# Optimization experiments

Measured on AMD Instinct MI355X. Metric: run time of the kernel, lower is better.

The kernel has to match this reference:

```python
import jax, jax.numpy as jnp
import numpy as np

B, N, C = 8, 196, 512
NC, H = 10, 8
HD = C // H
SCALE = HD ** -0.5


def setup_inputs() -> dict:
    key = jax.random.key(0)
    ks = jax.random.split(key, 8)
    s = 1.0 / np.sqrt(C)
    return {
        "x": jax.random.normal(ks[0], (B, N, C), jnp.float32),
        "anchors": jax.random.normal(ks[1], (NC, N, C), jnp.float32),
        "weights": jax.random.uniform(ks[2], (B, H, NC), jnp.float32),
        "Wqk": jax.random.normal(ks[3], (C, C), jnp.float32) * s,
        "Wqk2": jax.random.normal(ks[4], (C, C), jnp.float32) * s,
        "Wv": jax.random.normal(ks[5], (C, C), jnp.float32) * s,
        "Wproj": jax.random.normal(ks[6], (C, C), jnp.float32) * s,
        "bproj": jax.random.normal(ks[7], (C,), jnp.float32) * 0.01,
    }


def _heads(t):
    # (..., N, C) -> (..., H, N, HD)
    shp = t.shape[:-2]
    return t.reshape(shp + (t.shape[-2], H, HD)).swapaxes(-3, -2)


def reference(x, anchors, weights, Wqk, Wqk2, Wv, Wproj, bproj):
    v = _heads(x @ Wv)                      # (B, H, N, HD)
    q = _heads(x @ Wqk)[:, None]            # (B, 1, H, N, HD)
    k = _heads(anchors @ Wqk)[None]         # (1, NC, H, N, HD)
    q2 = _heads(x @ Wqk2)[:, None]          # (B, 1, H, N, HD)
    k2 = _heads(anchors @ Wqk2)[None]       # (1, NC, H, N, HD)

    # ReLU-clipped double attention, both (B, NC, H, N, N)
    left_attn = jnp.maximum(-(q @ k.swapaxes(-2, -1)) * SCALE, 0.0)
    right_attn = jnp.maximum((k2 @ q2.swapaxes(-2, -1)) * SCALE, 0.0)

    attn = left_attn @ right_attn           # (B, NC, H, N, N)
    # per-head class-weighted combine: (B,H,NC) x (B,NC,H,N,N) -> (B,H,N,N)
    tmp = jnp.einsum('bhc,bchnm->bhnm', weights, attn)
    out = tmp @ v                           # (B, H, N, HD)
    # NOTE: original torch code reshapes (B,H,N,HD)->(B,N,C) WITHOUT a
    # transpose back; we replicate that exact flatten order.
    out = out.reshape(B, N, C)
    out = out @ Wproj + bproj
    return (out, left_attn)
```

## Files before the change

kernel.cpp:

```cpp
#include <hip/hip_runtime.h>

#define OFF_XB     0u
#define OFF_AB     1605632u
#define OFF_WQKT   3612672u
#define OFF_WQK2T  4136960u
#define OFF_WVT    4661248u
#define OFF_WPROJT 5185536u
#define OFF_XQ     5709824u
#define OFF_XQ2    7315456u
#define OFF_AQ     8921088u
#define OFF_AQ2    10928128u
#define OFF_XVT    12935168u
#define OFF_WRVT   14639104u
#define OFF_OUT1   36265984u

typedef __attribute__((ext_vector_type(8))) short bf16x8;
typedef __attribute__((ext_vector_type(4))) float f32x4;
#define MFMA(a, b, c) __builtin_amdgcn_mfma_f32_16x16x32_bf16((a), (b), (c), 0, 0, 0)

__device__ __forceinline__ unsigned short f2bf(float x) {
  unsigned u = __builtin_bit_cast(unsigned, x);
  u += 0x7fffu + ((u >> 16) & 1u);
  return (unsigned short)(u >> 16);
}

__device__ __forceinline__ void gl_lds16(const void* g, void* l) {
  __builtin_amdgcn_global_load_lds(
      (const __attribute__((address_space(1))) unsigned int*)g,
      (__attribute__((address_space(3))) unsigned int*)l, 16, 0, 0);
}

__device__ __forceinline__ void stage128(const unsigned short* g0, int stride,
                                         unsigned short (*T)[72], int tid) {
  char* base = (char*)&T[0][0];
  int wv = tid >> 6;
#pragma unroll
  for (int i = 0; i < 4; i++) {
    int k = i * 256 + tid;
    int r = k / 9, c = k - r * 9;
    gl_lds16(g0 + (size_t)r * stride + (c << 3), base + (((i << 2) + wv) << 10));
  }
  if (tid < 128) {
    int k = 1024 + tid;
    int r = k / 9, c = k - r * 9;
    gl_lds16(g0 + (size_t)r * stride + (c << 3), base + ((16 + wv) << 10));
  }
}

__device__ __forceinline__ void stage64x128(const unsigned short* g0, int stride,
                                            unsigned short (*T)[136], int tid) {
  char* base = (char*)&T[0][0];
  int wv = tid >> 6;
#pragma unroll
  for (int i = 0; i < 4; i++) {
    int k = i * 256 + tid;
    int r = k / 17, c = k - r * 17;
    gl_lds16(g0 + (size_t)r * stride + (c << 3), base + (((i << 2) + wv) << 10));
  }
  if (tid < 64) {
    int k = 1024 + tid;
    int r = k / 17, c = k - r * 17;
    gl_lds16(g0 + (size_t)r * stride + (c << 3), base + (16 << 10));
  }
}

__device__ __forceinline__ void stage64(const unsigned short* g0, int stride,
                                        unsigned short (*T)[72], int tid) {
  int wv = tid >> 6;
  char* base = (char*)&T[0][0];
#pragma unroll
  for (int i = 0; i < 2; i++) {
    int k = i * 256 + tid;
    int r = k / 9, c = k - r * 9;
    gl_lds16(g0 + (size_t)r * stride + (c << 3), base + (((i << 2) + wv) << 10));
  }
  if (tid < 64) {
    int k = 512 + tid;
    int r = k / 9, c = k - r * 9;
    gl_lds16(g0 + (size_t)r * stride + (c << 3), base + 8192);
  }
}

__global__ __launch_bounds__(256) void pre_kernel(const float* __restrict__ x, const float* __restrict__ anchors,
                                                  const float* __restrict__ Wqk, const float* __restrict__ Wqk2,
                                                  const float* __restrict__ Wv, const float* __restrict__ Wproj,
                                                  char* __restrict__ ws) {
  int tid = threadIdx.x;
  if (blockIdx.x < 1764) {
    int base = blockIdx.x * 1024 + (tid << 2);
    float4 f = (base < 802816) ? *(const float4*)(x + base)
                               : *(const float4*)(anchors + (base - 802816));
    unsigned short s[4] = {f2bf(f.x), f2bf(f.y), f2bf(f.z), f2bf(f.w)};
    *(uint2*)((unsigned short*)(ws + OFF_XB) + base) = *(uint2*)s;
    return;
  }
  __shared__ unsigned short Ls[64][72];
  int idx = blockIdx.x - 1764;
  int wsel = idx >> 6, t = idx & 63;
  int k0 = (t >> 3) << 6, n0 = (t & 7) << 6;
  const float* W;
  unsigned short* WT;
  switch (wsel) {
    case 0:  W = Wqk;   WT = (unsigned short*)(ws + OFF_WQKT);   break;
    case 1:  W = Wqk2;  WT = (unsigned short*)(ws + OFF_WQK2T);  break;
    case 2:  W = Wv;    WT = (unsigned short*)(ws + OFF_WVT);    break;
    default: W = Wproj; WT = (unsigned short*)(ws + OFF_WPROJT); break;
  }
  {
    int r = tid >> 2, seg = (tid & 3) << 4;
    const float* p = W + (size_t)(k0 + r) * 512 + n0 + seg;
    float4 f0 = *(const float4*)p, f1 = *(const float4*)(p + 4);
    float4 f2 = *(const float4*)(p + 8), f3 = *(const float4*)(p + 12);
    unsigned short s[16] = {f2bf(f0.x), f2bf(f0.y), f2bf(f0.z), f2bf(f0.w),
                            f2bf(f1.x), f2bf(f1.y), f2bf(f1.z), f2bf(f1.w),
                            f2bf(f2.x), f2bf(f2.y), f2bf(f2.z), f2bf(f2.w),
                            f2bf(f3.x), f2bf(f3.y), f2bf(f3.z), f2bf(f3.w)};
    *(uint4*)&Ls[r][seg] = *(uint4*)s;
    *(uint4*)&Ls[r][seg + 8] = *(uint4*)(s + 8);
  }
  __syncthreads();
  {
    int r = tid >> 2, seg = (tid & 3) << 4;
    unsigned short s[16];
#pragma unroll
    for (int u = 0; u < 16; u++) s[u] = Ls[seg + u][r];
    unsigned short* dst = WT + (size_t)(n0 + r) * 512 + k0 + seg;
    *(uint4*)dst = *(uint4*)s;
    *(uint4*)(dst + 8) = *(uint4*)(s + 8);
  }
}

__global__ __launch_bounds__(256) void proj5(char* __restrict__ ws) {
  __shared__ unsigned short As[128][72];
  __shared__ unsigned short Bsh[128][72];
  const unsigned short* A;
  const unsigned short* Bp;
  unsigned short* O;
  int M, ostride, row0, col0;
  int z = blockIdx.z;
  if (z < 4) {
    row0 = blockIdx.x << 7;
    col0 = blockIdx.y << 7;
    ostride = 512;
    if (z < 2) { A = (const unsigned short*)(ws + OFF_XB); M = 1568; if (blockIdx.x >= 13) return; }
    else       { A = (const unsigned short*)(ws + OFF_AB); M = 1960; }
    Bp = (const unsigned short*)(ws + ((z & 1) ? OFF_WQK2T : OFF_WQKT));
    O  = (unsigned short*)(ws + (z == 0 ? OFF_XQ : z == 1 ? OFF_XQ2 : z == 2 ? OFF_AQ : OFF_AQ2));
  } else {
    if (blockIdx.x >= 13) return;
    row0 = blockIdx.y << 7;
    col0 = blockIdx.x << 7;
    A = (const unsigned short*)(ws + OFF_WVT);
    Bp = (const unsigned short*)(ws + OFF_XB);
    O = (unsigned short*)(ws + OFF_XVT);
    M = 512; ostride = 1664;
  }
  int tid = threadIdx.x;
  int w = tid >> 6, lm = tid & 15, lq = (tid >> 4) & 3;
  int h1 = w & 1, h2 = w >> 1;
  f32x4 acc[4][4] = {};
  for (int k0 = 0; k0 < 512; k0 += 64) {
    __syncthreads();
    stage128(A + (size_t)row0 * 512 + k0, 512, As, tid);
    stage128(Bp + (size_t)col0 * 512 + k0, 512, Bsh, tid);
    __syncthreads();
#pragma unroll
    for (int kk = 0; kk < 2; kk++) {
      bf16x8 bfr[4];
#pragma unroll
      for (int ni = 0; ni < 4; ni++)
        bfr[ni] = *(const bf16x8*)&Bsh[(h2 << 6) + (ni << 4) + lm][(kk << 5) + (lq << 3)];
#pragma unroll
      for (int mi = 0; mi < 4; mi++) {
        bf16x8 afr = *(const bf16x8*)&As[(h1 << 6) + (mi << 4) + lm][(kk << 5) + (lq << 3)];
#pragma unroll
        for (int ni = 0; ni < 4; ni++) acc[mi][ni] = MFMA(afr, bfr[ni], acc[mi][ni]);
      }
    }
  }
#pragma unroll
  for (int mi = 0; mi < 4; mi++)
#pragma unroll
    for (int r = 0; r < 4; r++) {
      int row = row0 + (h1 << 6) + (mi << 4) + (lq << 2) + r;
      if (row < M) {
#pragma unroll
        for (int ni = 0; ni < 4; ni++) {
          int col = col0 + (h2 << 6) + (ni << 4) + lm;
          O[(size_t)row * ostride + col] = f2bf(acc[mi][ni][r]);
        }
      }
    }
}

__global__ __launch_bounds__(256) void rv2(char* __restrict__ ws, const float* __restrict__ weights) {
  const unsigned short* xq2 = (const unsigned short*)(ws + OFF_XQ2);
  const unsigned short* aq2 = (const unsigned short*)(ws + OFF_AQ2);
  const unsigned short* xvt = (const unsigned short*)(ws + OFF_XVT);
  unsigned short* wrvt      = (unsigned short*)(ws + OFF_WRVT);
  __shared__ unsigned short Bs[128][72];
  __shared__ unsigned short Ss[128][136];
  __shared__ unsigned short Vt[64][136];
  int jblk = blockIdx.x, bch = blockIdx.y;
  int h = bch & 7, bc = bch >> 3;
  int c = bc % 10, b = bc / 10;
  int bh = b * 8 + h;
  int tid = threadIdx.x;
  int w = tid >> 6, lm = tid & 15, lq = (tid >> 4) & 3;
  int h1 = w & 1, h2 = w >> 1;
  float wc = weights[bh * 10 + c];

  stage128(aq2 + (size_t)(c * 196 + jblk * 128) * 512 + (h << 6), 512, Bs, tid);
  __syncthreads();
  bf16x8 af[4][2];
#pragma unroll
  for (int mi = 0; mi < 4; mi++)
#pragma unroll
    for (int kk = 0; kk < 2; kk++)
      af[mi][kk] = *(const bf16x8*)&Bs[(h1 << 6) + (mi << 4) + lm][(kk << 5) + (lq << 3)];

  f32x4 acc[4][2] = {};
  for (int mt = 0; mt < 2; mt++) {
    __syncthreads();
    stage128(xq2 + (size_t)(b * 196 + mt * 128) * 512 + (h << 6), 512, Bs, tid);
    stage64x128(xvt + (size_t)(h << 6) * 1664 + b * 196 + mt * 128, 1664, Vt, tid);
    __syncthreads();
    f32x4 s[4][4] = {};
#pragma unroll
    for (int kk = 0; kk < 2; kk++) {
      bf16x8 bfr[4];
#pragma unroll
      for (int ni = 0; ni < 4; ni++)
        bfr[ni] = *(const bf16x8*)&Bs[(h2 << 6) + (ni << 4) + lm][(kk << 5) + (lq << 3)];
#pragma unroll
      for (int mi = 0; mi < 4; mi++)
#pragma unroll
        for (int ni = 0; ni < 4; ni++) s[mi][ni] = MFMA(af[mi][kk], bfr[ni], s[mi][ni]);
    }
#pragma unroll
    for (int ni = 0; ni < 4; ni++) {
      int ml = (h2 << 6) + (ni << 4) + lm;
      bool ok = (mt * 128 + ml) < 196;
#pragma unroll
      for (int mi = 0; mi < 4; mi++)
#pragma unroll
        for (int r = 0; r < 4; r++) {
          float v = ok ? fmaxf(0.125f * s[mi][ni][r], 0.f) : 0.f;
          Ss[(h1 << 6) + (mi << 4) + (lq << 2) + r][ml] = f2bf(v);
        }
    }
    __syncthreads();
#pragma unroll
    for (int kk = 0; kk < 4; kk++) {
      bf16x8 bfr[2];
#pragma unroll
      for (int ni = 0; ni < 2; ni++)
        bfr[ni] = *(const bf16x8*)&Vt[(h2 << 5) + (ni << 4) + lm][(kk << 5) + (lq << 3)];
#pragma unroll
      for (int mi = 0; mi < 4; mi++) {
        bf16x8 afr = *(const bf16x8*)&Ss[(h1 << 6) + (mi << 4) + lm][(kk << 5) + (lq << 3)];
#pragma unroll
        for (int ni = 0; ni < 2; ni++) acc[mi][ni] = MFMA(afr, bfr[ni], acc[mi][ni]);
      }
    }
  }
  __syncthreads();
#pragma unroll
  for (int mi = 0; mi < 4; mi++)
#pragma unroll
    for (int ni = 0; ni < 2; ni++)
#pragma unroll
      for (int r = 0; r < 4; r++)
        Ss[(h2 << 5) + (ni << 4) + lm][(h1 << 6) + (mi << 4) + (lq << 2) + r] =
            f2bf(wc * acc[mi][ni][r]);
  __syncthreads();
  {
    int dd = tid >> 2, seg = (tid & 3) << 5;
    unsigned short vbuf[32];
#pragma unroll
    for (int u = 0; u < 32; u++) {
      int j = jblk * 128 + seg + u;
      vbuf[u] = (j < 196) ? Ss[dd][seg + u] : (unsigned short)0;
    }
    unsigned short* dst = wrvt + ((size_t)bch * 64 + dd) * 264 + jblk * 128 + seg;
#pragma unroll
    for (int u = 0; u < 4; u++) *(uint4*)(dst + (u << 3)) = *(uint4*)&vbuf[u << 3];
  }
}

__global__ __launch_bounds__(256) void attn_left(char* __restrict__ ws, float* __restrict__ left,
                                                 float* __restrict__ out1) {
  const unsigned short* xq   = (const unsigned short*)(ws + OFF_XQ);
  const unsigned short* aq   = (const unsigned short*)(ws + OFF_AQ);
  const unsigned short* wrvt = (const unsigned short*)(ws + OFF_WRVT);
  __shared__ unsigned short Bs[128][72];
  __shared__ unsigned short Ss[128][136];
  __shared__ unsigned short Rt[64][136];
  int iblk = blockIdx.x, bch = blockIdx.y;
  int h = bch & 7, bc = bch >> 3;
  int c = bc % 10, b = bc / 10;
  int bh = b * 8 + h;
  int tid = threadIdx.x;
  int w = tid >> 6, lm = tid & 15, lq = (tid >> 4) & 3;
  int h1 = w & 1, h2 = w >> 1;

  stage128(xq + (size_t)(b * 196 + iblk * 128) * 512 + (h << 6), 512, Bs, tid);
  __syncthreads();
  bf16x8 qf[4][2];
#pragma unroll
  for (int mi = 0; mi < 4; mi++)
#pragma unroll
    for (int kk = 0; kk < 2; kk++)
      qf[mi][kk] = *(const bf16x8*)&Bs[(h1 << 6) + (mi << 4) + lm][(kk << 5) + (lq << 3)];

  f32x4 acc[4][2] = {};
  size_t lbase = (size_t)bch * (196 * 196);
  for (int jt = 0; jt < 2; jt++) {
    __syncthreads();
    stage128(aq + (size_t)(c * 196 + jt * 128) * 512 + (h << 6), 512, Bs, tid);
    stage64x128(wrvt + (size_t)bch * 64 * 264 + jt * 128, 264, Rt, tid);
    __syncthreads();
    f32x4 s[4][4] = {};
#pragma unroll
    for (int kk = 0; kk < 2; kk++) {
      bf16x8 bfr[4];
#pragma unroll
      for (int ni = 0; ni < 4; ni++)
        bfr[ni] = *(const bf16x8*)&Bs[(h2 << 6) + (ni << 4) + lm][(kk << 5) + (lq << 3)];
#pragma unroll
      for (int mi = 0; mi < 4; mi++)
#pragma unroll
        for (int ni = 0; ni < 4; ni++) s[mi][ni] = MFMA(qf[mi][kk], bfr[ni], s[mi][ni]);
    }
#pragma unroll
    for (int mi = 0; mi < 4; mi++)
#pragma unroll
      for (int r = 0; r < 4; r++) {
        int il = (h1 << 6) + (mi << 4) + (lq << 2) + r;
        int i = iblk * 128 + il;
        bool iok = i < 196;
#pragma unroll
        for (int ni = 0; ni < 4; ni++) {
          int jl = (h2 << 6) + (ni << 4) + lm;
          float v = fmaxf(-0.125f * s[mi][ni][r], 0.f);
          Ss[il][jl] = f2bf(v);
          int j = jt * 128 + jl;
          if (iok && j < 196) left[lbase + (size_t)i * 196 + j] = v;
        }
      }
    __syncthreads();
#pragma unroll
    for (int kk = 0; kk < 4; kk++) {
      bf16x8 bfr[2];
#pragma unroll
      for (int ni = 0; ni < 2; ni++)
        bfr[ni] = *(const bf16x8*)&Rt[(h2 << 5) + (ni << 4) + lm][(kk << 5) + (lq << 3)];
#pragma unroll
      for (int mi = 0; mi < 4; mi++) {
        bf16x8 afr = *(const bf16x8*)&Ss[(h1 << 6) + (mi << 4) + lm][(kk << 5) + (lq << 3)];
#pragma unroll
        for (int ni = 0; ni < 2; ni++) acc[mi][ni] = MFMA(afr, bfr[ni], acc[mi][ni]);
      }
    }
  }
#pragma unroll
  for (int mi = 0; mi < 4; mi++)
#pragma unroll
    for (int r = 0; r < 4; r++) {
      int i = iblk * 128 + (h1 << 6) + (mi << 4) + (lq << 2) + r;
      if (i < 196) {
#pragma unroll
        for (int ni = 0; ni < 2; ni++) {
          int dd = (h2 << 5) + (ni << 4) + lm;
          atomicAdd(&out1[((size_t)bh * 196 + i) * 64 + dd], acc[mi][ni][r]);
        }
      }
    }
}

__global__ __launch_bounds__(256) void final_gemm(const float* __restrict__ A, const unsigned short* __restrict__ WT,
                                                  const float* __restrict__ bias, float* __restrict__ out) {
  __shared__ unsigned short As[64][72];
  __shared__ unsigned short Ws[64][72];
  int row0 = blockIdx.x << 6;
  int col0 = blockIdx.y << 6;
  int tid = threadIdx.x;
  int w = tid >> 6, lm = tid & 15, lq = (tid >> 4) & 3;
  f32x4 acc[4] = {};
  for (int k0 = 0; k0 < 512; k0 += 64) {
    __syncthreads();
    {
      int r = tid >> 2, c0 = (tid & 3) << 4;
      float4 f0, f1, f2, f3;
      if (row0 + r < 1568) {
        const float* p = A + (size_t)(row0 + r) * 512 + k0 + c0;
        f0 = *(const float4*)p;       f1 = *(const float4*)(p + 4);
        f2 = *(const float4*)(p + 8); f3 = *(const float4*)(p + 12);
      } else {
        f0 = f1 = f2 = f3 = make_float4(0.f, 0.f, 0.f, 0.f);
      }
      unsigned short s[16] = {f2bf(f0.x), f2bf(f0.y), f2bf(f0.z), f2bf(f0.w),
                              f2bf(f1.x), f2bf(f1.y), f2bf(f1.z), f2bf(f1.w),
                              f2bf(f2.x), f2bf(f2.y), f2bf(f2.z), f2bf(f2.w),
                              f2bf(f3.x), f2bf(f3.y), f2bf(f3.z), f2bf(f3.w)};
      *(uint4*)&As[r][c0] = *(uint4*)s;
      *(uint4*)&As[r][c0 + 8] = *(uint4*)(s + 8);
    }
    stage64(WT + (size_t)col0 * 512 + k0, 512, Ws, tid);
    __syncthreads();
#pragma unroll
    for (int kk = 0; kk < 2; kk++) {
      bf16x8 bf = *(const bf16x8*)&Ws[(w << 4) + lm][(kk << 5) + (lq << 3)];
#pragma unroll
      for (int mi = 0; mi < 4; mi++) {
        bf16x8 af = *(const bf16x8*)&As[(mi << 4) + lm][(kk << 5) + (lq << 3)];
        acc[mi] = MFMA(af, bf, acc[mi]);
      }
    }
  }
  int ncol = col0 + (w << 4) + lm;
  float bv = bias[ncol];
#pragma unroll
  for (int mi = 0; mi < 4; mi++)
#pragma unroll
    for (int r2 = 0; r2 < 4; r2++) {
      int row = row0 + (mi << 4) + (lq << 2) + r2;
      if (row < 1568) out[(size_t)row * 512 + ncol] = acc[mi][r2] + bv;
    }
}

extern "C" void kernel_launch(void* const* d_in, const int* in_sizes, int n_in,
                              void* d_out, int out_size, void* d_ws, size_t ws_size,
                              hipStream_t stream) {
  (void)in_sizes; (void)n_in; (void)out_size; (void)ws_size;
  const float* x       = (const float*)d_in[0];
  const float* anchors = (const float*)d_in[1];
  const float* weights = (const float*)d_in[2];
  const float* Wqk     = (const float*)d_in[3];
  const float* Wqk2    = (const float*)d_in[4];
  const float* Wv      = (const float*)d_in[5];
  const float* Wproj   = (const float*)d_in[6];
  const float* bproj   = (const float*)d_in[7];
  char* ws = (char*)d_ws;
  float* out  = (float*)d_out;
  float* left = out + 802816;
  float* out1 = (float*)(ws + OFF_OUT1);

  dim3 blk(256);
  hipMemsetAsync(out1, 0, 3211264, stream);
  pre_kernel<<<dim3(2020), blk, 0, stream>>>(x, anchors, Wqk, Wqk2, Wv, Wproj, ws);
  proj5<<<dim3(16, 4, 5), blk, 0, stream>>>(ws);
  rv2<<<dim3(2, 640), blk, 0, stream>>>(ws, weights);
  attn_left<<<dim3(2, 640), blk, 0, stream>>>(ws, left, out1);
  final_gemm<<<dim3(25, 8), blk, 0, stream>>>(out1, (const unsigned short*)(ws + OFF_WPROJT), bproj, out);
}
```

Measured before the change: 235.5 us.

## Load MFMA operands directly from global memory instead of LDS staging

Removes the LDS staging (global_load_lds tiles plus syncthreads) in proj5, rv2 and attn_left, so each lane now loads its bf16x8 MFMA fragments straight from global memory. The V-transpose buffer is also re-laid out per batch with a 208-column stride, and proj5's grid mapping and column masking change to match. This is meant to cut LDS traffic, barriers and LDS footprint, raising occupancy, at the cost of redundant, less coalesced global and L2 reads across waves.

```diff
diff --git a/kernel.cpp b/kernel.cpp
--- a/kernel.cpp
+++ b/kernel.cpp
@@ -30,40 +30,6 @@
       (__attribute__((address_space(3))) unsigned int*)l, 16, 0, 0);
 }
 
-__device__ __forceinline__ void stage128(const unsigned short* g0, int stride,
-                                         unsigned short (*T)[72], int tid) {
-  char* base = (char*)&T[0][0];
-  int wv = tid >> 6;
-#pragma unroll
-  for (int i = 0; i < 4; i++) {
-    int k = i * 256 + tid;
-    int r = k / 9, c = k - r * 9;
-    gl_lds16(g0 + (size_t)r * stride + (c << 3), base + (((i << 2) + wv) << 10));
-  }
-  if (tid < 128) {
-    int k = 1024 + tid;
-    int r = k / 9, c = k - r * 9;
-    gl_lds16(g0 + (size_t)r * stride + (c << 3), base + ((16 + wv) << 10));
-  }
-}
-
-__device__ __forceinline__ void stage64x128(const unsigned short* g0, int stride,
-                                            unsigned short (*T)[136], int tid) {
-  char* base = (char*)&T[0][0];
-  int wv = tid >> 6;
-#pragma unroll
-  for (int i = 0; i < 4; i++) {
-    int k = i * 256 + tid;
-    int r = k / 17, c = k - r * 17;
-    gl_lds16(g0 + (size_t)r * stride + (c << 3), base + (((i << 2) + wv) << 10));
-  }
-  if (tid < 64) {
-    int k = 1024 + tid;
-    int r = k / 17, c = k - r * 17;
-    gl_lds16(g0 + (size_t)r * stride + (c << 3), base + (16 << 10));
-  }
-}
-
 __device__ __forceinline__ void stage64(const unsigned short* g0, int stride,
                                         unsigned short (*T)[72], int tid) {
   int wv = tid >> 6;
@@ -131,52 +97,51 @@
 }
 
 __global__ __launch_bounds__(256) void proj5(char* __restrict__ ws) {
-  __shared__ unsigned short As[128][72];
-  __shared__ unsigned short Bsh[128][72];
-  const unsigned short* A;
-  const unsigned short* Bp;
+  const unsigned short *A, *Bp;
   unsigned short* O;
-  int M, ostride, row0, col0;
+  int M, Nmask, ostride, row0, col0;
   int z = blockIdx.z;
   if (z < 4) {
+    if (z < 2 && blockIdx.x >= 13) return;
     row0 = blockIdx.x << 7;
     col0 = blockIdx.y << 7;
-    ostride = 512;
-    if (z < 2) { A = (const unsigned short*)(ws + OFF_XB); M = 1568; if (blockIdx.x >= 13) return; }
-    else       { A = (const unsigned short*)(ws + OFF_AB); M = 1960; }
+    ostride = 512; Nmask = 512;
+    A = (const unsigned short*)(ws + (z < 2 ? OFF_XB : OFF_AB));
+    M = (z < 2) ? 1568 : 1960;
     Bp = (const unsigned short*)(ws + ((z & 1) ? OFF_WQK2T : OFF_WQKT));
-    O  = (unsigned short*)(ws + (z == 0 ? OFF_XQ : z == 1 ? OFF_XQ2 : z == 2 ? OFF_AQ : OFF_AQ2));
+    O = (unsigned short*)(ws + (z == 0 ? OFF_XQ : z == 1 ? OFF_XQ2 : z == 2 ? OFF_AQ : OFF_AQ2));
   } else {
-    if (blockIdx.x >= 13) return;
+    int b = blockIdx.x >> 1;
     row0 = blockIdx.y << 7;
-    col0 = blockIdx.x << 7;
+    col0 = (blockIdx.x & 1) << 7;
     A = (const unsigned short*)(ws + OFF_WVT);
-    Bp = (const unsigned short*)(ws + OFF_XB);
-    O = (unsigned short*)(ws + OFF_XVT);
-    M = 512; ostride = 1664;
+    Bp = (const unsigned short*)(ws + OFF_XB) + (size_t)(b * 196) * 512;
+    O = (unsigned short*)(ws + OFF_XVT) + (size_t)b * 512 * 208;
+    M = 512; Nmask = 208; ostride = 208;
   }
   int tid = threadIdx.x;
   int w = tid >> 6, lm = tid & 15, lq = (tid >> 4) & 3;
   int h1 = w & 1, h2 = w >> 1;
+  const unsigned short* ar[4];
+  const unsigned short* br[4];
+#pragma unroll
+  for (int mi = 0; mi < 4; mi++)
+    ar[mi] = A + (size_t)(row0 + (h1 << 6) + (mi << 4) + lm) * 512 + (lq << 3);
+#pragma unroll
+  for (int ni = 0; ni < 4; ni++)
+    br[ni] = Bp + (size_t)(col0 + (h2 << 6) + (ni << 4) + lm) * 512 + (lq << 3);
   f32x4 acc[4][4] = {};
-  for (int k0 = 0; k0 < 512; k0 += 64) {
-    __syncthreads();
-    stage128(A + (size_t)row0 * 512 + k0, 512, As, tid);
-    stage128(Bp + (size_t)col0 * 512 + k0, 512, Bsh, tid);
-    __syncthreads();
-#pragma unroll
-    for (int kk = 0; kk < 2; kk++) {
-      bf16x8 bfr[4];
-#pragma unroll
-      for (int ni = 0; ni < 4; ni++)
-        bfr[ni] = *(const bf16x8*)&Bsh[(h2 << 6) + (ni << 4) + lm][(kk << 5) + (lq << 3)];
-#pragma unroll
-      for (int mi = 0; mi < 4; mi++) {
-        bf16x8 afr = *(const bf16x8*)&As[(h1 << 6) + (mi << 4) + lm][(kk << 5) + (lq << 3)];
-#pragma unroll
-        for (int ni = 0; ni < 4; ni++) acc[mi][ni] = MFMA(afr, bfr[ni], acc[mi][ni]);
-      }
-    }
+#pragma unroll 4
+  for (int kk = 0; kk < 16; kk++) {
+    bf16x8 bfr[4], afr[4];
+#pragma unroll
+    for (int ni = 0; ni < 4; ni++) bfr[ni] = *(const bf16x8*)(br[ni] + (kk << 5));
+#pragma unroll
+    for (int mi = 0; mi < 4; mi++) afr[mi] = *(const bf16x8*)(ar[mi] + (kk << 5));
+#pragma unroll
+    for (int mi = 0; mi < 4; mi++)
+#pragma unroll
+      for (int ni = 0; ni < 4; ni++) acc[mi][ni] = MFMA(afr[mi], bfr[ni], acc[mi][ni]);
   }
 #pragma unroll
   for (int mi = 0; mi < 4; mi++)
@@ -187,7 +152,7 @@
 #pragma unroll
         for (int ni = 0; ni < 4; ni++) {
           int col = col0 + (h2 << 6) + (ni << 4) + lm;
-          O[(size_t)row * ostride + col] = f2bf(acc[mi][ni][r]);
+          if (col < Nmask) O[(size_t)row * ostride + col] = f2bf(acc[mi][ni][r]);
         }
       }
     }
@@ -198,9 +163,7 @@
   const unsigned short* aq2 = (const unsigned short*)(ws + OFF_AQ2);
   const unsigned short* xvt = (const unsigned short*)(ws + OFF_XVT);
   unsigned short* wrvt      = (unsigned short*)(ws + OFF_WRVT);
-  __shared__ unsigned short Bs[128][72];
   __shared__ unsigned short Ss[128][136];
-  __shared__ unsigned short Vt[64][136];
   int jblk = blockIdx.x, bch = blockIdx.y;
   int h = bch & 7, bc = bch >> 3;
   int c = bc % 10, b = bc / 10;
@@ -209,38 +172,38 @@
   int w = tid >> 6, lm = tid & 15, lq = (tid >> 4) & 3;
   int h1 = w & 1, h2 = w >> 1;
   float wc = weights[bh * 10 + c];
-
-  stage128(aq2 + (size_t)(c * 196 + jblk * 128) * 512 + (h << 6), 512, Bs, tid);
-  __syncthreads();
-  bf16x8 af[4][2];
-#pragma unroll
-  for (int mi = 0; mi < 4; mi++)
-#pragma unroll
-    for (int kk = 0; kk < 2; kk++)
-      af[mi][kk] = *(const bf16x8*)&Bs[(h1 << 6) + (mi << 4) + lm][(kk << 5) + (lq << 3)];
+  int ja0 = jblk << 7;
+
+  bf16x8 kf[4][2];
+#pragma unroll
+  for (int mi = 0; mi < 4; mi++) {
+    const unsigned short* p =
+        aq2 + (size_t)(c * 196 + ja0 + (h1 << 6) + (mi << 4) + lm) * 512 + (h << 6) + (lq << 3);
+#pragma unroll
+    for (int kk = 0; kk < 2; kk++) kf[mi][kk] = *(const bf16x8*)(p + (kk << 5));
+  }
 
   f32x4 acc[4][2] = {};
   for (int mt = 0; mt < 2; mt++) {
-    __syncthreads();
-    stage128(xq2 + (size_t)(b * 196 + mt * 128) * 512 + (h << 6), 512, Bs, tid);
-    stage64x128(xvt + (size_t)(h << 6) * 1664 + b * 196 + mt * 128, 1664, Vt, tid);
-    __syncthreads();
+    int m0 = mt << 7;
     f32x4 s[4][4] = {};
 #pragma unroll
     for (int kk = 0; kk < 2; kk++) {
       bf16x8 bfr[4];
 #pragma unroll
       for (int ni = 0; ni < 4; ni++)
-        bfr[ni] = *(const bf16x8*)&Bs[(h2 << 6) + (ni << 4) + lm][(kk << 5) + (lq << 3)];
+        bfr[ni] = *(const bf16x8*)(xq2 +
+            (size_t)(b * 196 + m0 + (h2 << 6) + (ni << 4) + lm) * 512 + (h << 6) + (kk << 5) + (lq << 3));
 #pragma unroll
       for (int mi = 0; mi < 4; mi++)
 #pragma unroll
-        for (int ni = 0; ni < 4; ni++) s[mi][ni] = MFMA(af[mi][kk], bfr[ni], s[mi][ni]);
-    }
+        for (int ni = 0; ni < 4; ni++) s[mi][ni] = MFMA(kf[mi][kk], bfr[ni], s[mi][ni]);
+    }
+    __syncthreads();
 #pragma unroll
     for (int ni = 0; ni < 4; ni++) {
       int ml = (h2 << 6) + (ni << 4) + lm;
-      bool ok = (mt * 128 + ml) < 196;
+      bool ok = (m0 + ml) < 196;
 #pragma unroll
       for (int mi = 0; mi < 4; mi++)
 #pragma unroll
@@ -251,14 +214,17 @@
     }
     __syncthreads();
 #pragma unroll
-    for (int kk = 0; kk < 4; kk++) {
+    for (int kkp = 0; kkp < 4; kkp++) {
       bf16x8 bfr[2];
 #pragma unroll
-      for (int ni = 0; ni < 2; ni++)
-        bfr[ni] = *(const bf16x8*)&Vt[(h2 << 5) + (ni << 4) + lm][(kk << 5) + (lq << 3)];
+      for (int ni = 0; ni < 2; ni++) {
+        int ddl = (h2 << 5) + (ni << 4) + lm;
+        bfr[ni] = *(const bf16x8*)(xvt +
+            ((size_t)(b * 512) + (h << 6) + ddl) * 208 + m0 + (kkp << 5) + (lq << 3));
+      }
 #pragma unroll
       for (int mi = 0; mi < 4; mi++) {
-        bf16x8 afr = *(const bf16x8*)&Ss[(h1 << 6) + (mi << 4) + lm][(kk << 5) + (lq << 3)];
+        bf16x8 afr = *(const bf16x8*)&Ss[(h1 << 6) + (mi << 4) + lm][(kkp << 5) + (lq << 3)];
 #pragma unroll
         for (int ni = 0; ni < 2; ni++) acc[mi][ni] = MFMA(afr, bfr[ni], acc[mi][ni]);
       }
@@ -279,10 +245,10 @@
     unsigned short vbuf[32];
 #pragma unroll
     for (int u = 0; u < 32; u++) {
-      int j = jblk * 128 + seg + u;
+      int j = ja0 + seg + u;
       vbuf[u] = (j < 196) ? Ss[dd][seg + u] : (unsigned short)0;
     }
-    unsigned short* dst = wrvt + ((size_t)bch * 64 + dd) * 264 + jblk * 128 + seg;
+    unsigned short* dst = wrvt + ((size_t)bch * 64 + dd) * 264 + ja0 + seg;
 #pragma unroll
     for (int u = 0; u < 4; u++) *(uint4*)(dst + (u << 3)) = *(uint4*)&vbuf[u << 3];
   }
@@ -293,9 +259,7 @@
   const unsigned short* xq   = (const unsigned short*)(ws + OFF_XQ);
   const unsigned short* aq   = (const unsigned short*)(ws + OFF_AQ);
   const unsigned short* wrvt = (const unsigned short*)(ws + OFF_WRVT);
-  __shared__ unsigned short Bs[128][72];
   __shared__ unsigned short Ss[128][136];
-  __shared__ unsigned short Rt[64][136];
   int iblk = blockIdx.x, bch = blockIdx.y;
   int h = bch & 7, bc = bch >> 3;
   int c = bc % 10, b = bc / 10;
@@ -303,61 +267,64 @@
   int tid = threadIdx.x;
   int w = tid >> 6, lm = tid & 15, lq = (tid >> 4) & 3;
   int h1 = w & 1, h2 = w >> 1;
-
-  stage128(xq + (size_t)(b * 196 + iblk * 128) * 512 + (h << 6), 512, Bs, tid);
-  __syncthreads();
+  int i0 = iblk << 7;
+
   bf16x8 qf[4][2];
 #pragma unroll
-  for (int mi = 0; mi < 4; mi++)
-#pragma unroll
-    for (int kk = 0; kk < 2; kk++)
-      qf[mi][kk] = *(const bf16x8*)&Bs[(h1 << 6) + (mi << 4) + lm][(kk << 5) + (lq << 3)];
+  for (int mi = 0; mi < 4; mi++) {
+    const unsigned short* p =
+        xq + (size_t)(b * 196 + i0 + (h1 << 6) + (mi << 4) + lm) * 512 + (h << 6) + (lq << 3);
+#pragma unroll
+    for (int kk = 0; kk < 2; kk++) qf[mi][kk] = *(const bf16x8*)(p + (kk << 5));
+  }
 
   f32x4 acc[4][2] = {};
   size_t lbase = (size_t)bch * (196 * 196);
   for (int jt = 0; jt < 2; jt++) {
-    __syncthreads();
-    stage128(aq + (size_t)(c * 196 + jt * 128) * 512 + (h << 6), 512, Bs, tid);
-    stage64x128(wrvt + (size_t)bch * 64 * 264 + jt * 128, 264, Rt, tid);
-    __syncthreads();
+    int j0 = jt << 7;
     f32x4 s[4][4] = {};
 #pragma unroll
     for (int kk = 0; kk < 2; kk++) {
       bf16x8 bfr[4];
 #pragma unroll
       for (int ni = 0; ni < 4; ni++)
-        bfr[ni] = *(const bf16x8*)&Bs[(h2 << 6) + (ni << 4) + lm][(kk << 5) + (lq << 3)];
+        bfr[ni] = *(const bf16x8*)(aq +
+            (size_t)(c * 196 + j0 + (h2 << 6) + (ni << 4) + lm) * 512 + (h << 6) + (kk << 5) + (lq << 3));
 #pragma unroll
       for (int mi = 0; mi < 4; mi++)
 #pragma unroll
         for (int ni = 0; ni < 4; ni++) s[mi][ni] = MFMA(qf[mi][kk], bfr[ni], s[mi][ni]);
     }
+    __syncthreads();
 #pragma unroll
     for (int mi = 0; mi < 4; mi++)
 #pragma unroll
       for (int r = 0; r < 4; r++) {
         int il = (h1 << 6) + (mi << 4) + (lq << 2) + r;
-        int i = iblk * 128 + il;
+        int i = i0 + il;
         bool iok = i < 196;
 #pragma unroll
         for (int ni = 0; ni < 4; ni++) {
           int jl = (h2 << 6) + (ni << 4) + lm;
           float v = fmaxf(-0.125f * s[mi][ni][r], 0.f);
           Ss[il][jl] = f2bf(v);
-          int j = jt * 128 + jl;
+          int j = j0 + jl;
           if (iok && j < 196) left[lbase + (size_t)i * 196 + j] = v;
         }
       }
     __syncthreads();
 #pragma unroll
-    for (int kk = 0; kk < 4; kk++) {
+    for (int kkp = 0; kkp < 4; kkp++) {
       bf16x8 bfr[2];
 #pragma unroll
-      for (int ni = 0; ni < 2; ni++)
-        bfr[ni] = *(const bf16x8*)&Rt[(h2 << 5) + (ni << 4) + lm][(kk << 5) + (lq << 3)];
+      for (int ni = 0; ni < 2; ni++) {
+        int ddl = (h2 << 5) + (ni << 4) + lm;
+        bfr[ni] = *(const bf16x8*)(wrvt +
+            ((size_t)bch * 64 + ddl) * 264 + j0 + (kkp << 5) + (lq << 3));
+      }
 #pragma unroll
       for (int mi = 0; mi < 4; mi++) {
-        bf16x8 afr = *(const bf16x8*)&Ss[(h1 << 6) + (mi << 4) + lm][(kk << 5) + (lq << 3)];
+        bf16x8 afr = *(const bf16x8*)&Ss[(h1 << 6) + (mi << 4) + lm][(kkp << 5) + (lq << 3)];
 #pragma unroll
         for (int ni = 0; ni < 2; ni++) acc[mi][ni] = MFMA(afr, bfr[ni], acc[mi][ni]);
       }
@@ -367,7 +334,7 @@
   for (int mi = 0; mi < 4; mi++)
 #pragma unroll
     for (int r = 0; r < 4; r++) {
-      int i = iblk * 128 + (h1 << 6) + (mi << 4) + (lq << 2) + r;
+      int i = i0 + (h1 << 6) + (mi << 4) + (lq << 2) + r;
       if (i < 196) {
 #pragma unroll
         for (int ni = 0; ni < 2; ni++) {
```

Result: slower. 258.0 us (+9.5%).
